# Kernel optimization log

Measured on AMD Instinct MI355X. Metric: run time of the kernel, lower is better.

The kernel has to match this reference:

```python
import jax, jax.numpy as jnp
import numpy as np

B, C, H, W = 8, 512, 32, 32
EMB, HEADS, GROUPS = 512, 8, 32
DH = EMB // HEADS
EPS = 1e-5


def setup_inputs() -> dict:
    key = jax.random.key(0)
    ks = jax.random.split(key, 11)
    s_in = 1.0 / np.sqrt(C)
    s_emb = 1.0 / np.sqrt(EMB)
    return {
        "x": jax.random.normal(ks[0], (B, C, H, W), jnp.float32),
        "Wq": jax.random.uniform(ks[1], (C, EMB), jnp.float32, -s_in, s_in),
        "bq": jax.random.uniform(ks[2], (EMB,), jnp.float32, -s_in, s_in),
        "Wk": jax.random.uniform(ks[3], (C, EMB), jnp.float32, -s_in, s_in),
        "bk": jax.random.uniform(ks[4], (EMB,), jnp.float32, -s_in, s_in),
        "Wv": jax.random.uniform(ks[5], (C, EMB), jnp.float32, -s_in, s_in),
        "bv": jax.random.uniform(ks[6], (EMB,), jnp.float32, -s_in, s_in),
        "Wo": jax.random.uniform(ks[7], (EMB, EMB), jnp.float32, -s_emb, s_emb),
        "bo": jax.random.uniform(ks[8], (EMB,), jnp.float32, -s_emb, s_emb),
        "gn_w": jnp.ones((EMB,), jnp.float32),
        "gn_b": jnp.zeros((EMB,), jnp.float32),
    }


def _group_norm(y, w, b):
    # y: [B, C, H, W]; normalize within each of GROUPS channel groups over (C//G, H, W)
    b_, c_, h_, w_ = y.shape
    yg = y.reshape(b_, GROUPS, c_ // GROUPS, h_, w_)
    mean = yg.mean(axis=(2, 3, 4), keepdims=True)
    var = yg.var(axis=(2, 3, 4), keepdims=True)
    yg = (yg - mean) * jax.lax.rsqrt(var + EPS)
    y = yg.reshape(b_, c_, h_, w_)
    return y * w[None, :, None, None] + b[None, :, None, None]


def reference(x, Wq, bq, Wk, bk, Wv, bv, Wo, bo, gn_w, gn_b):
    b, c, h, w = x.shape
    s = h * w
    xs = x.reshape(b, c, s).transpose(0, 2, 1)  # [B, S, C]
    # QKV projections, split into heads: [B, heads, S, dh]
    def heads(t):
        return t.reshape(b, s, HEADS, DH).transpose(0, 2, 1, 3)
    q = heads(xs @ Wq + bq)
    k = heads(xs @ Wk + bk)
    v = heads(xs @ Wv + bv)
    scale = DH ** -0.5
    scores = jnp.einsum('bhqd,bhkd->bhqk', q, k) * scale  # [B, heads, S, S]
    attn = jax.nn.softmax(scores, axis=-1)
    out = jnp.einsum('bhqk,bhkd->bhqd', attn, v)  # [B, heads, S, dh]
    out = out.transpose(0, 2, 1, 3).reshape(b, s, EMB)  # concat heads
    proj = out @ Wo + bo  # [B, S, EMB]
    proj = proj.transpose(0, 2, 1).reshape(b, EMB, h, w)
    return _group_norm(proj + x, gn_w, gn_b)
```

## Files before the change

### kernel.cpp

```cpp
#include <hip/hip_runtime.h>

#define BB 8
#define CC 512
#define SS 1024
#define EMB 512
#define HEADS 8
#define DH 64
#define GROUPS 32
#define CPG 16
#define EPS 1e-5f

typedef __bf16 bf16x8 __attribute__((ext_vector_type(8)));
typedef __bf16 bf16x4 __attribute__((ext_vector_type(4)));
typedef float f32x4 __attribute__((ext_vector_type(4)));
typedef unsigned short u16x4 __attribute__((ext_vector_type(4)));

__device__ inline unsigned short f2bf(float f) {
    union { float f; unsigned u; } c; c.f = f;
    unsigned u = c.u + 0x7FFF + ((c.u >> 16) & 1);
    return (unsigned short)(u >> 16);
}

#if defined(__has_builtin)
#if __has_builtin(__builtin_amdgcn_exp2f)
#define EXP2F(x) __builtin_amdgcn_exp2f(x)
#endif
#endif
#ifndef EXP2F
#define EXP2F(x) __expf(0.69314718f * (x))
#endif

#define MFMA16(a, b, c) __builtin_amdgcn_mfma_f32_16x16x32_bf16((a), (b), (c), 0, 0, 0)
#define GLOAD_LDS16(g, s)                                                     \
    __builtin_amdgcn_global_load_lds(                                         \
        (const __attribute__((address_space(1))) void*)(g),                   \
        (__attribute__((address_space(3))) void*)(s), 16, 0, 0)

__global__ __launch_bounds__(256) void prep_x(
    const float* __restrict__ x, unsigned short* __restrict__ xT)
{
    __shared__ float tile[32][33];
    const int s0 = blockIdx.x * 32;
    const int c0 = blockIdx.y * 32;
    const int b  = blockIdx.z;
    const int t  = threadIdx.x;

    {
        int c = t >> 3, s4 = (t & 7) * 4;
        float4 v = *(const float4*)(x + ((size_t)b * CC + c0 + c) * SS + s0 + s4);
        tile[c][s4] = v.x; tile[c][s4 + 1] = v.y;
        tile[c][s4 + 2] = v.z; tile[c][s4 + 3] = v.w;
    }
    __syncthreads();
    {
        int sr = t >> 3, c4 = (t & 7) * 4;
        u16x4 o;
        #pragma unroll
        for (int i = 0; i < 4; ++i) o[i] = f2bf(tile[c4 + i][sr]);
        *(u16x4*)(xT + ((size_t)(b << 10) + s0 + sr) * CC + c0 + c4) = o;
    }
}

__global__ __launch_bounds__(256) void prep_w(
    const float* __restrict__ Wq, const float* __restrict__ Wk,
    const float* __restrict__ Wv, const float* __restrict__ Wo,
    unsigned short* __restrict__ Wt)
{
    __shared__ float tile[32][33];
    const int z = blockIdx.z;
    const float* W = (z == 0) ? Wq : (z == 1) ? Wk : (z == 2) ? Wv : Wo;
    unsigned short* dst = Wt + (size_t)z * EMB * CC;
    const int k0 = blockIdx.x * 32;
    const int n0 = blockIdx.y * 32;
    const int t  = threadIdx.x;

    {
        int k = t >> 3, n4 = (t & 7) * 4;
        float4 v = *(const float4*)(W + (size_t)(k0 + k) * EMB + n0 + n4);
        tile[k][n4] = v.x; tile[k][n4 + 1] = v.y;
        tile[k][n4 + 2] = v.z; tile[k][n4 + 3] = v.w;
    }
    __syncthreads();
    {
        int n = t >> 3, k4 = (t & 7) * 4;
        u16x4 o;
        #pragma unroll
        for (int i = 0; i < 4; ++i) o[i] = f2bf(tile[k4 + i][n]);
        *(u16x4*)(dst + (size_t)(n0 + n) * CC + k0 + k4) = o;
    }
}

#define GEMM_CORE(Aptr, Bptr)                                                  \
    __shared__ __align__(16) char lds[32768];                                  \
    const int t = threadIdx.x, w = t >> 6, l = t & 63;                         \
    const int wr = w >> 1, wc = w & 1;                                         \
    const int rl = l & 15, kh = l >> 4;                                        \
    f32x4 acc[4][4] = {};                                                      \
    {                                                                          \
        const int srow = w * 32 + (l >> 2);                                    \
        const int sslot = (l & 3) ^ ((srow >> 1) & 3);                         \
        const char* Ag0 = (const char*)(Aptr) + (size_t)(m0 + srow) * 1024 + sslot * 16;      \
        const char* Ag1 = (const char*)(Aptr) + (size_t)(m0 + srow + 16) * 1024 + (((l & 3) ^ (((srow + 16) >> 1) & 3)) * 16); \
        const char* Bg0 = (const char*)(Bptr) + (size_t)(n0 + srow) * 1024 + sslot * 16;      \
        const char* Bg1 = (const char*)(Bptr) + (size_t)(n0 + srow + 16) * 1024 + (((l & 3) ^ (((srow + 16) >> 1) & 3)) * 16); \
        for (int kt = 0; kt < 16; ++kt) {                                      \
            if (kt == 0) {                                                     \
                GLOAD_LDS16(Ag0, lds + w * 2048);                              \
                GLOAD_LDS16(Ag1, lds + w * 2048 + 1024);                       \
                GLOAD_LDS16(Bg0, lds + 8192 + w * 2048);                       \
                GLOAD_LDS16(Bg1, lds + 8192 + w * 2048 + 1024);                \
                __syncthreads();                                               \
            }                                                                  \
            const int buf = kt & 1;                                            \
            if (kt < 15) {                                                     \
                const int kb = (kt + 1) * 64;                                  \
                char* Al = lds + (buf ^ 1) * 16384;                            \
                char* Bl = Al + 8192;                                          \
                GLOAD_LDS16(Ag0 + kb, Al + w * 2048);                          \
                GLOAD_LDS16(Ag1 + kb, Al + w * 2048 + 1024);                   \
                GLOAD_LDS16(Bg0 + kb, Bl + w * 2048);                          \
                GLOAD_LDS16(Bg1 + kb, Bl + w * 2048 + 1024);                   \
            }                                                                  \
            const char* Al = lds + buf * 16384;                                \
            const char* Bl = Al + 8192;                                        \
            bf16x8 af[4], bfr[4];                                              \
            _Pragma("unroll")                                                  \
            for (int i = 0; i < 4; ++i) {                                      \
                int row = wr * 64 + i * 16 + rl;                               \
                af[i] = *(const bf16x8*)(Al + row * 64 + ((kh ^ ((row >> 1) & 3)) << 4)); \
                int col = wc * 64 + i * 16 + rl;                               \
                bfr[i] = *(const bf16x8*)(Bl + col * 64 + ((kh ^ ((col >> 1) & 3)) << 4)); \
            }                                                                  \
            _Pragma("unroll")                                                  \
            for (int i = 0; i < 4; ++i)                                        \
                _Pragma("unroll")                                              \
                for (int j = 0; j < 4; ++j)                                    \
                    acc[i][j] = MFMA16(af[i], bfr[j], acc[i][j]);              \
            __syncthreads();                                                   \
        }                                                                      \
    }

__global__ __launch_bounds__(256) void qkv_mm(
    const unsigned short* __restrict__ xT, const unsigned short* __restrict__ Wt,
    const float* __restrict__ bq, const float* __restrict__ bk,
    const float* __restrict__ bv,
    unsigned short* __restrict__ Qb, unsigned short* __restrict__ Kb,
    unsigned short* __restrict__ Vb)
{
    const int z = blockIdx.z;
    const unsigned short* Bt = Wt + (size_t)z * EMB * CC;
    const float* bias = (z == 0) ? bq : (z == 1) ? bk : bv;
    const int m0 = blockIdx.x * 128, n0 = blockIdx.y * 128;

    GEMM_CORE(xT, Bt)

    if (z == 2) {
        #pragma unroll
        for (int i = 0; i < 4; ++i) {
            #pragma unroll
            for (int j = 0; j < 4; ++j) {
                int n = n0 + wc * 64 + j * 16 + rl;
                int h = n >> 6, d = n & 63;
                float bi = bias[n];
                int mb = m0 + wr * 64 + i * 16 + kh * 4;
                int b = mb >> 10, s = mb & 1023;
                bf16x4 o;
                #pragma unroll
                for (int r = 0; r < 4; ++r) o[r] = (__bf16)(acc[i][j][r] + bi);
                *(bf16x4*)((__bf16*)Vb + (((size_t)(b * HEADS + h)) * DH + d) * SS + s) = o;
            }
        }
    } else {
        unsigned short* outp = (z == 0) ? Qb : Kb;
        #pragma unroll
        for (int i = 0; i < 4; ++i) {
            #pragma unroll
            for (int j = 0; j < 4; ++j) {
                int n = n0 + wc * 64 + j * 16 + rl;
                int h = n >> 6, d = n & 63;
                float bi = bias[n];
                #pragma unroll
                for (int r = 0; r < 4; ++r) {
                    int m = m0 + wr * 64 + i * 16 + kh * 4 + r;
                    int b = m >> 10, s = m & 1023;
                    ((__bf16*)outp)[(((size_t)(b * HEADS + h)) * SS + s) * DH + d] =
                        (__bf16)(acc[i][j][r] + bi);
                }
            }
        }
    }
}

__global__ __launch_bounds__(256) void proj_mm(
    const unsigned short* __restrict__ AO, const unsigned short* __restrict__ Wot,
    const float* __restrict__ bo, const float* __restrict__ x,
    float* __restrict__ Y)
{
    const int m0 = blockIdx.x * 128, n0 = blockIdx.y * 128;

    GEMM_CORE(AO, Wot)

    #pragma unroll
    for (int i = 0; i < 4; ++i) {
        #pragma unroll
        for (int j = 0; j < 4; ++j) {
            int n = n0 + wc * 64 + j * 16 + rl;
            float bi = bo[n];
            int mb = m0 + wr * 64 + i * 16 + kh * 4;
            int b = mb >> 10, s = mb & 1023;
            const float4 xr = *(const float4*)(x + ((size_t)b * CC + n) * SS + s);
            float4 o;
            o.x = acc[i][j][0] + bi + xr.x;
            o.y = acc[i][j][1] + bi + xr.y;
            o.z = acc[i][j][2] + bi + xr.z;
            o.w = acc[i][j][3] + bi + xr.w;
            *(float4*)(Y + ((size_t)b * CC + n) * SS + s) = o;
        }
    }
}

__global__ __launch_bounds__(256) void attn_mfma(
    const unsigned short* __restrict__ Q, const unsigned short* __restrict__ K,
    const unsigned short* __restrict__ V, unsigned short* __restrict__ Aout)
{
    __shared__ __align__(16) char lds[49152];

    const int wg  = blockIdx.x;
    const int xcd = wg & 7;
    const int idx = wg >> 3;
    const int pair = xcd * 8 + (idx >> 3);
    const int qb   = idx & 7;
    const int h = pair & 7;
    const int b = pair >> 3;
    const int q0 = qb * 128;

    const size_t kbase = ((size_t)b * HEADS + h) * SS * DH;
    const size_t vbase = ((size_t)b * HEADS + h) * DH * SS;

    const int t  = threadIdx.x;
    const int w  = t >> 6;
    const int l  = t & 63;
    const int g  = l >> 4;
    const int qi = l & 15;
    char* Pl = lds + 32768 + w * 4096;

    bf16x8 qf[2][2];
    #pragma unroll
    for (int u = 0; u < 2; ++u) {
        const unsigned short* qrow =
            Q + kbase + (size_t)(q0 + w * 32 + u * 16 + qi) * DH;
        qf[u][0] = *(const bf16x8*)(qrow + g * 8);
        qf[u][1] = *(const bf16x8*)(qrow + 32 + g * 8);
    }

    const int srow = t >> 3;
    const int seg  = t & 7;
    const unsigned short* kg0 = K + kbase + (size_t)srow * DH + ((seg ^ (srow & 7)) * 8);
    const unsigned short* vg0 = V + vbase + (size_t)srow * SS + ((seg ^ (srow & 7)) * 8);

#define ATTN_STAGE(bb, ktn)                                                    \
    GLOAD_LDS16(kg0 + (ktn) * 4096, lds + (bb) + t * 16);                      \
    GLOAD_LDS16(kg0 + (ktn) * 4096 + 2048, lds + (bb) + 4096 + t * 16);        \
    GLOAD_LDS16(vg0 + (ktn) * 64, lds + (bb) + 8192 + t * 16);                 \
    GLOAD_LDS16(vg0 + (ktn) * 64 + 32768, lds + (bb) + 12288 + t * 16);

    f32x4 O[4][2] = {};
    float m2[2]   = {-1e30f, -1e30f};
    float lsum[2] = {0.f, 0.f};
    const float cscale = 0.125f * 1.44269504f;

    int bufb = 0;
    ATTN_STAGE(0, 0)
    __syncthreads();

    for (int kt = 0; kt < 16; ++kt) {
        if (kt < 15) { ATTN_STAGE(bufb ^ 16384, kt + 1) }

        const char* Kl = lds + bufb;
        const char* Vl = lds + bufb + 8192;

        f32x4 st[4][2] = {};
        __builtin_amdgcn_s_setprio(1);
        #pragma unroll
        for (int tt = 0; tt < 4; ++tt) {
            int row = tt * 16 + qi;
            bf16x8 kf0 = *(const bf16x8*)(Kl + row * 128 +
                          ((g * 16) ^ ((row & 7) << 4)));
            bf16x8 kf1 = *(const bf16x8*)(Kl + row * 128 +
                          ((64 + g * 16) ^ ((row & 7) << 4)));
            #pragma unroll
            for (int u = 0; u < 2; ++u) {
                st[tt][u] = MFMA16(kf0, qf[u][0], st[tt][u]);
                st[tt][u] = MFMA16(kf1, qf[u][1], st[tt][u]);
            }
        }
        __builtin_amdgcn_s_setprio(0);

        float pmax[2] = {-1e30f, -1e30f};
        #pragma unroll
        for (int tt = 0; tt < 4; ++tt)
            #pragma unroll
            for (int u = 0; u < 2; ++u)
                #pragma unroll
                for (int r = 0; r < 4; ++r) {
                    float v = st[tt][u][r] * cscale;
                    st[tt][u][r] = v;
                    pmax[u] = fmaxf(pmax[u], v);
                }
        #pragma unroll
        for (int u = 0; u < 2; ++u) {
            if (!__all(pmax[u] <= m2[u] + 8.0f)) {
                float gm = fmaxf(pmax[u], __shfl_xor(pmax[u], 16));
                gm = fmaxf(gm, __shfl_xor(gm, 32));
                float newm = fmaxf(m2[u], gm);
                float alpha = EXP2F(m2[u] - newm);
                #pragma unroll
                for (int dt = 0; dt < 4; ++dt)
                    #pragma unroll
                    for (int r = 0; r < 4; ++r) O[dt][u][r] *= alpha;
                lsum[u] *= alpha;
                m2[u] = newm;
            }
            #pragma unroll
            for (int tt = 0; tt < 4; ++tt) {
                bf16x4 pk;
                #pragma unroll
                for (int r = 0; r < 4; ++r) {
                    float p = EXP2F(st[tt][u][r] - m2[u]);
                    lsum[u] += p;
                    pk[r] = (__bf16)p;
                }
                *(bf16x4*)(Pl + u * 2048 + qi * 128 +
                           ((tt * 32 + g * 8) ^ ((qi & 7) << 4))) = pk;
            }
        }

        bf16x8 pf[2][2];
        #pragma unroll
        for (int u = 0; u < 2; ++u)
            #pragma unroll
            for (int hh = 0; hh < 2; ++hh)
                pf[u][hh] = *(const bf16x8*)(Pl + u * 2048 + qi * 128 +
                             ((hh * 64 + g * 16) ^ ((qi & 7) << 4)));
        __builtin_amdgcn_s_setprio(1);
        #pragma unroll
        for (int dt = 0; dt < 4; ++dt) {
            int d = dt * 16 + qi;
            bf16x8 vf0 = *(const bf16x8*)(Vl + d * 128 + ((g * 16) ^ ((d & 7) << 4)));
            bf16x8 vf1 = *(const bf16x8*)(Vl + d * 128 + ((64 + g * 16) ^ ((d & 7) << 4)));
            #pragma unroll
            for (int u = 0; u < 2; ++u) {
                O[dt][u] = MFMA16(vf0, pf[u][0], O[dt][u]);
                O[dt][u] = MFMA16(vf1, pf[u][1], O[dt][u]);
            }
        }
        __builtin_amdgcn_s_setprio(0);

        __syncthreads();
        bufb ^= 16384;
    }

    #pragma unroll
    for (int u = 0; u < 2; ++u) {
        float ls = lsum[u];
        ls += __shfl_xor(ls, 16);
        ls += __shfl_xor(ls, 32);
        const float inv = __builtin_amdgcn_rcpf(ls);
        unsigned short* orow = Aout +
            ((size_t)b * SS + q0 + w * 32 + u * 16 + qi) * EMB + h * DH;
        #pragma unroll
        for (int dt = 0; dt < 4; ++dt) {
            bf16x4 o;
            #pragma unroll
            for (int r = 0; r < 4; ++r) o[r] = (__bf16)(O[dt][u][r] * inv);
            *(bf16x4*)((__bf16*)orow + dt * 16 + g * 4) = o;
        }
    }
#undef ATTN_STAGE
}

__global__ __launch_bounds__(256) void gnorm2(
    const float* __restrict__ Y, const float* __restrict__ gw,
    const float* __restrict__ gb, float* __restrict__ out)
{
    __shared__ float red[8];
    __shared__ float stats[2];

    const int grp = blockIdx.x;
    const int b   = blockIdx.y;
    const int t   = threadIdx.x;
    const size_t base = ((size_t)b * CC + grp * CPG) * SS;

    float sum = 0.f, sq = 0.f;
    #pragma unroll
    for (int i = 0; i < 16; ++i) {
        float4 v = *(const float4*)(Y + base + (size_t)(t + i * 256) * 4);
        sum += v.x + v.y + v.z + v.w;
        sq  += v.x * v.x + v.y * v.y + v.z * v.z + v.w * v.w;
    }
    #pragma unroll
    for (int off = 32; off; off >>= 1) {
        sum += __shfl_down(sum, off);
        sq  += __shfl_down(sq, off);
    }
    const int wid = t >> 6;
    if ((t & 63) == 0) { red[wid] = sum; red[4 + wid] = sq; }
    __syncthreads();
    if (t == 0) {
        float s1 = red[0] + red[1] + red[2] + red[3];
        float s2 = red[4] + red[5] + red[6] + red[7];
        float mean = s1 / (float)(CPG * SS);
        float var  = s2 / (float)(CPG * SS) - mean * mean;
        stats[0] = mean;
        stats[1] = rsqrtf(var + EPS);
    }
    __syncthreads();
    const float mean = stats[0], rs = stats[1];

    #pragma unroll
    for (int i = 0; i < 16; ++i) {
        size_t idx = (size_t)(t + i * 256) * 4;
        int ch = grp * CPG + (int)(idx >> 10);
        float wgt = gw[ch], bet = gb[ch];
        float4 v = *(const float4*)(Y + base + idx);
        float4 o;
        o.x = (v.x - mean) * rs * wgt + bet;
        o.y = (v.y - mean) * rs * wgt + bet;
        o.z = (v.z - mean) * rs * wgt + bet;
        o.w = (v.w - mean) * rs * wgt + bet;
        *(float4*)(out + base + idx) = o;
    }
}

extern "C" void kernel_launch(void* const* d_in, const int* in_sizes, int n_in,
                              void* d_out, int out_size, void* d_ws, size_t ws_size,
                              hipStream_t stream) {
    const float* x   = (const float*)d_in[0];
    const float* Wq  = (const float*)d_in[1];
    const float* bq  = (const float*)d_in[2];
    const float* Wk  = (const float*)d_in[3];
    const float* bk  = (const float*)d_in[4];
    const float* Wv  = (const float*)d_in[5];
    const float* bv  = (const float*)d_in[6];
    const float* Wo  = (const float*)d_in[7];
    const float* bo  = (const float*)d_in[8];
    const float* gnw = (const float*)d_in[9];
    const float* gnb = (const float*)d_in[10];
    float* out = (float*)d_out;
    char* ws  = (char*)d_ws;

    unsigned short* xT  = (unsigned short*)(ws);
    unsigned short* Wt  = (unsigned short*)(ws + 8388608);
    unsigned short* Qb  = (unsigned short*)(ws + 10485760);
    unsigned short* Kb  = (unsigned short*)(ws + 18874368);
    unsigned short* Vb  = (unsigned short*)(ws + 27262976);
    unsigned short* AO  = (unsigned short*)(ws + 35651584);
    float*          Y   = (float*)(ws + 44040192);

    prep_x<<<dim3(32, 16, 8), 256, 0, stream>>>(x, xT);
    prep_w<<<dim3(16, 16, 4), 256, 0, stream>>>(Wq, Wk, Wv, Wo, Wt);
    qkv_mm<<<dim3(64, 4, 3), 256, 0, stream>>>(xT, Wt, bq, bk, bv, Qb, Kb, Vb);
    attn_mfma<<<dim3(512), 256, 0, stream>>>(Qb, Kb, Vb, AO);
    proj_mm<<<dim3(64, 4), 256, 0, stream>>>(AO, Wt + (size_t)3 * EMB * CC, bo, x, Y);
    gnorm2<<<dim3(32, 8), 256, 0, stream>>>(Y, gnw, gnb, out);
}
```

Before: 87.10 us.

## Merge prep kernels, fold softmax scale into Q, store residual sum as bf16

```diff
diff --git a/kernel.cpp b/kernel.cpp
--- a/kernel.cpp
+++ b/kernel.cpp
@@ -36,57 +36,55 @@
         (const __attribute__((address_space(1))) void*)(g),                   \
         (__attribute__((address_space(3))) void*)(s), 16, 0, 0)
 
-__global__ __launch_bounds__(256) void prep_x(
-    const float* __restrict__ x, unsigned short* __restrict__ xT)
+__global__ __launch_bounds__(256) void prep_all(
+    const float* __restrict__ x,
+    const float* __restrict__ Wq, const float* __restrict__ Wk,
+    const float* __restrict__ Wv, const float* __restrict__ Wo,
+    unsigned short* __restrict__ xT, unsigned short* __restrict__ Wt)
 {
     __shared__ float tile[32][33];
-    const int s0 = blockIdx.x * 32;
-    const int c0 = blockIdx.y * 32;
-    const int b  = blockIdx.z;
-    const int t  = threadIdx.x;
-
-    {
-        int c = t >> 3, s4 = (t & 7) * 4;
-        float4 v = *(const float4*)(x + ((size_t)b * CC + c0 + c) * SS + s0 + s4);
-        tile[c][s4] = v.x; tile[c][s4 + 1] = v.y;
-        tile[c][s4 + 2] = v.z; tile[c][s4 + 3] = v.w;
-    }
-    __syncthreads();
-    {
-        int sr = t >> 3, c4 = (t & 7) * 4;
-        u16x4 o;
-        #pragma unroll
-        for (int i = 0; i < 4; ++i) o[i] = f2bf(tile[c4 + i][sr]);
-        *(u16x4*)(xT + ((size_t)(b << 10) + s0 + sr) * CC + c0 + c4) = o;
-    }
-}
-
-__global__ __launch_bounds__(256) void prep_w(
-    const float* __restrict__ Wq, const float* __restrict__ Wk,
-    const float* __restrict__ Wv, const float* __restrict__ Wo,
-    unsigned short* __restrict__ Wt)
-{
-    __shared__ float tile[32][33];
-    const int z = blockIdx.z;
-    const float* W = (z == 0) ? Wq : (z == 1) ? Wk : (z == 2) ? Wv : Wo;
-    unsigned short* dst = Wt + (size_t)z * EMB * CC;
-    const int k0 = blockIdx.x * 32;
-    const int n0 = blockIdx.y * 32;
-    const int t  = threadIdx.x;
-
-    {
-        int k = t >> 3, n4 = (t & 7) * 4;
-        float4 v = *(const float4*)(W + (size_t)(k0 + k) * EMB + n0 + n4);
-        tile[k][n4] = v.x; tile[k][n4 + 1] = v.y;
-        tile[k][n4 + 2] = v.z; tile[k][n4 + 3] = v.w;
-    }
-    __syncthreads();
-    {
-        int n = t >> 3, k4 = (t & 7) * 4;
-        u16x4 o;
-        #pragma unroll
-        for (int i = 0; i < 4; ++i) o[i] = f2bf(tile[k4 + i][n]);
-        *(u16x4*)(dst + (size_t)(n0 + n) * CC + k0 + k4) = o;
+    const int t = threadIdx.x;
+
+    if (blockIdx.x < 4096) {
+        const int i  = blockIdx.x;
+        const int s0 = (i & 31) * 32;
+        const int c0 = ((i >> 5) & 15) * 32;
+        const int b  = i >> 9;
+        {
+            int c = t >> 3, s4 = (t & 7) * 4;
+            float4 v = *(const float4*)(x + ((size_t)b * CC + c0 + c) * SS + s0 + s4);
+            tile[c][s4] = v.x; tile[c][s4 + 1] = v.y;
+            tile[c][s4 + 2] = v.z; tile[c][s4 + 3] = v.w;
+        }
+        __syncthreads();
+        {
+            int sr = t >> 3, c4 = (t & 7) * 4;
+            u16x4 o;
+            #pragma unroll
+            for (int i2 = 0; i2 < 4; ++i2) o[i2] = f2bf(tile[c4 + i2][sr]);
+            *(u16x4*)(xT + ((size_t)(b << 10) + s0 + sr) * CC + c0 + c4) = o;
+        }
+    } else {
+        const int i  = blockIdx.x - 4096;
+        const int k0 = (i & 15) * 32;
+        const int n0 = ((i >> 4) & 15) * 32;
+        const int z  = i >> 8;
+        const float* W = (z == 0) ? Wq : (z == 1) ? Wk : (z == 2) ? Wv : Wo;
+        unsigned short* dst = Wt + (size_t)z * EMB * CC;
+        {
+            int k = t >> 3, n4 = (t & 7) * 4;
+            float4 v = *(const float4*)(W + (size_t)(k0 + k) * EMB + n0 + n4);
+            tile[k][n4] = v.x; tile[k][n4 + 1] = v.y;
+            tile[k][n4 + 2] = v.z; tile[k][n4 + 3] = v.w;
+        }
+        __syncthreads();
+        {
+            int n = t >> 3, k4 = (t & 7) * 4;
+            u16x4 o;
+            #pragma unroll
+            for (int i2 = 0; i2 < 4; ++i2) o[i2] = f2bf(tile[k4 + i2][n]);
+            *(u16x4*)(dst + (size_t)(n0 + n) * CC + k0 + k4) = o;
+        }
     }
 }
 
@@ -172,6 +170,7 @@
         }
     } else {
         unsigned short* outp = (z == 0) ? Qb : Kb;
+        const float qs = (z == 0) ? 0.1803368801f : 1.0f;
         #pragma unroll
         for (int i = 0; i < 4; ++i) {
             #pragma unroll
@@ -184,7 +183,7 @@
                     int m = m0 + wr * 64 + i * 16 + kh * 4 + r;
                     int b = m >> 10, s = m & 1023;
                     ((__bf16*)outp)[(((size_t)(b * HEADS + h)) * SS + s) * DH + d] =
-                        (__bf16)(acc[i][j][r] + bi);
+                        (__bf16)((acc[i][j][r] + bi) * qs);
                 }
             }
         }
@@ -194,7 +193,7 @@
 __global__ __launch_bounds__(256) void proj_mm(
     const unsigned short* __restrict__ AO, const unsigned short* __restrict__ Wot,
     const float* __restrict__ bo, const float* __restrict__ x,
-    float* __restrict__ Y)
+    unsigned short* __restrict__ Yb)
 {
     const int m0 = blockIdx.x * 128, n0 = blockIdx.y * 128;
 
@@ -209,12 +208,12 @@
             int mb = m0 + wr * 64 + i * 16 + kh * 4;
             int b = mb >> 10, s = mb & 1023;
             const float4 xr = *(const float4*)(x + ((size_t)b * CC + n) * SS + s);
-            float4 o;
-            o.x = acc[i][j][0] + bi + xr.x;
-            o.y = acc[i][j][1] + bi + xr.y;
-            o.z = acc[i][j][2] + bi + xr.z;
-            o.w = acc[i][j][3] + bi + xr.w;
-            *(float4*)(Y + ((size_t)b * CC + n) * SS + s) = o;
+            bf16x4 o;
+            o[0] = (__bf16)(acc[i][j][0] + bi + xr.x);
+            o[1] = (__bf16)(acc[i][j][1] + bi + xr.y);
+            o[2] = (__bf16)(acc[i][j][2] + bi + xr.z);
+            o[3] = (__bf16)(acc[i][j][3] + bi + xr.w);
+            *(bf16x4*)((__bf16*)Yb + ((size_t)b * CC + n) * SS + s) = o;
         }
     }
 }
@@ -267,7 +266,6 @@
     f32x4 O[4][2] = {};
     float m2[2]   = {-1e30f, -1e30f};
     float lsum[2] = {0.f, 0.f};
-    const float cscale = 0.125f * 1.44269504f;
 
     int bufb = 0;
     ATTN_STAGE(0, 0)
@@ -302,11 +300,8 @@
             #pragma unroll
             for (int u = 0; u < 2; ++u)
                 #pragma unroll
-                for (int r = 0; r < 4; ++r) {
-                    float v = st[tt][u][r] * cscale;
-                    st[tt][u][r] = v;
-                    pmax[u] = fmaxf(pmax[u], v);
-                }
+                for (int r = 0; r < 4; ++r)
+                    pmax[u] = fmaxf(pmax[u], st[tt][u][r]);
         #pragma unroll
         for (int u = 0; u < 2; ++u) {
             if (!__all(pmax[u] <= m2[u] + 8.0f)) {
@@ -379,10 +374,11 @@
 #undef ATTN_STAGE
 }
 
-__global__ __launch_bounds__(256) void gnorm2(
-    const float* __restrict__ Y, const float* __restrict__ gw,
+__global__ __launch_bounds__(256) void gnorm3(
+    const __bf16* __restrict__ Yb, const float* __restrict__ gw,
     const float* __restrict__ gb, float* __restrict__ out)
 {
+    __shared__ __align__(16) __bf16 ybuf[CPG * SS];
     __shared__ float red[8];
     __shared__ float stats[2];
 
@@ -390,13 +386,19 @@
     const int b   = blockIdx.y;
     const int t   = threadIdx.x;
     const size_t base = ((size_t)b * CC + grp * CPG) * SS;
+    const __bf16* src = Yb + base;
 
     float sum = 0.f, sq = 0.f;
     #pragma unroll
-    for (int i = 0; i < 16; ++i) {
-        float4 v = *(const float4*)(Y + base + (size_t)(t + i * 256) * 4);
-        sum += v.x + v.y + v.z + v.w;
-        sq  += v.x * v.x + v.y * v.y + v.z * v.z + v.w * v.w;
+    for (int i = 0; i < 8; ++i) {
+        int off = i * 2048 + t * 8;
+        bf16x8 v = *(const bf16x8*)(src + off);
+        *(bf16x8*)(ybuf + off) = v;
+        #pragma unroll
+        for (int j = 0; j < 8; ++j) {
+            float f = (float)v[j];
+            sum += f; sq += f * f;
+        }
     }
     #pragma unroll
     for (int off = 32; off; off >>= 1) {
@@ -418,17 +420,18 @@
     const float mean = stats[0], rs = stats[1];
 
     #pragma unroll
-    for (int i = 0; i < 16; ++i) {
-        size_t idx = (size_t)(t + i * 256) * 4;
-        int ch = grp * CPG + (int)(idx >> 10);
-        float wgt = gw[ch], bet = gb[ch];
-        float4 v = *(const float4*)(Y + base + idx);
-        float4 o;
-        o.x = (v.x - mean) * rs * wgt + bet;
-        o.y = (v.y - mean) * rs * wgt + bet;
-        o.z = (v.z - mean) * rs * wgt + bet;
-        o.w = (v.w - mean) * rs * wgt + bet;
-        *(float4*)(out + base + idx) = o;
+    for (int i = 0; i < 8; ++i) {
+        int off = i * 2048 + t * 8;
+        int ch = grp * CPG + (off >> 10);
+        float wgt = gw[ch] * rs, bet = gb[ch] - mean * rs * gw[ch];
+        bf16x8 v = *(const bf16x8*)(ybuf + off);
+        float4 o0, o1;
+        o0.x = (float)v[0] * wgt + bet; o0.y = (float)v[1] * wgt + bet;
+        o0.z = (float)v[2] * wgt + bet; o0.w = (float)v[3] * wgt + bet;
+        o1.x = (float)v[4] * wgt + bet; o1.y = (float)v[5] * wgt + bet;
+        o1.z = (float)v[6] * wgt + bet; o1.w = (float)v[7] * wgt + bet;
+        *(float4*)(out + base + off)     = o0;
+        *(float4*)(out + base + off + 4) = o1;
     }
 }
 
@@ -455,12 +458,11 @@
     unsigned short* Kb  = (unsigned short*)(ws + 18874368);
     unsigned short* Vb  = (unsigned short*)(ws + 27262976);
     unsigned short* AO  = (unsigned short*)(ws + 35651584);
-    float*          Y   = (float*)(ws + 44040192);
-
-    prep_x<<<dim3(32, 16, 8), 256, 0, stream>>>(x, xT);
-    prep_w<<<dim3(16, 16, 4), 256, 0, stream>>>(Wq, Wk, Wv, Wo, Wt);
+    unsigned short* Yb  = (unsigned short*)(ws + 44040192);
+
+    prep_all<<<dim3(5120), 256, 0, stream>>>(x, Wq, Wk, Wv, Wo, xT, Wt);
     qkv_mm<<<dim3(64, 4, 3), 256, 0, stream>>>(xT, Wt, bq, bk, bv, Qb, Kb, Vb);
     attn_mfma<<<dim3(512), 256, 0, stream>>>(Qb, Kb, Vb, AO);
-    proj_mm<<<dim3(64, 4), 256, 0, stream>>>(AO, Wt + (size_t)3 * EMB * CC, bo, x, Y);
-    gnorm2<<<dim3(32, 8), 256, 0, stream>>>(Y, gnw, gnb, out);
-}
+    proj_mm<<<dim3(64, 4), 256, 0, stream>>>(AO, Wt + (size_t)3 * EMB * CC, bo, x, Yb);
+    gnorm3<<<dim3(32, 8), 256, 0, stream>>>((const __bf16*)Yb, gnw, gnb, out);
+}
```

After: 83.18 us. 1.05x faster.
